# Optimization experiments

Measured on AMD Instinct MI355X. Metric: run time of the kernel, lower is better.

Reference implementation:

```python
import jax, jax.numpy as jnp
import numpy as np
import math

# ---- module hyperparams (from init_kwargs) ----
L = 10            # number of hash-grid levels
DIM = 4           # features per level
LOG2T = 16
T = 1 << LOG2T    # hash table size per level
BASE = 16         # base resolution
PLS = 2.0         # per_level_scale
SCALE_MULTI = 0.5
HID = 64
IN_DIM = L * DIM  # 40
OUT_DIM = 13      # 1 + 12
N = 1_000_000

# growth factor b = exp((ln(finest) - ln(base)) / (L - 1)), finest = base * pls**L
B_GROWTH = math.exp((math.log(BASE * PLS ** L) - math.log(BASE)) / (L - 1))
RES = [int(math.floor(BASE * B_GROWTH ** l)) for l in range(L)]

PRIMES = np.array([1, 2654435761, 805459861], dtype=np.uint32)
# 8 corner offsets of a voxel
OFFS = np.array([[i, j, k] for i in (0, 1) for j in (0, 1) for k in (0, 1)], dtype=np.uint32)


def _hash_coords(c):
    # c: uint32 [N, 8, 3] -> int32 [N, 8] indices into table of size T
    p = jnp.asarray(PRIMES)
    h = (c[..., 0] * p[0]) ^ (c[..., 1] * p[1]) ^ (c[..., 2] * p[2])
    return (h & jnp.uint32(T - 1)).astype(jnp.int32)


def _encode(x, tables):
    # x: [N,3] in [0,1]; tables: [L, T, DIM] -> [N, DIM, L]
    offs_u = jnp.asarray(OFFS)                      # uint32 [8,3]
    offs_b = jnp.asarray(OFFS.astype(bool))         # bool   [8,3]
    feats = []
    for l in range(L):
        xs = x * RES[l]
        bottom = jnp.floor(xs)
        frac = xs - bottom                          # [N,3]
        corners = bottom.astype(jnp.uint32)[:, None, :] + offs_u[None]  # [N,8,3]
        idx = _hash_coords(corners)                 # [N,8]
        cf = tables[l][idx]                         # [N,8,DIM] gather
        # trilinear weights: prod over dims of frac (if offset==1) else (1-frac)
        w = jnp.prod(jnp.where(offs_b[None], frac[:, None, :], 1.0 - frac[:, None, :]), axis=-1)  # [N,8]
        feats.append(jnp.einsum('nc,ncd->nd', w, cf))  # [N,DIM]
    return jnp.stack(feats, axis=-1)                # [N, DIM, L]


def setup_inputs() -> dict:
    key = jax.random.key(0)
    ks = jax.random.split(key, 10)
    x = jax.random.uniform(ks[0], (N, 3), dtype=jnp.float32)
    cr = jax.random.uniform(ks[1], (N,), dtype=jnp.float32)
    tables = jax.random.uniform(ks[2], (L, T, DIM), dtype=jnp.float32, minval=-1e-4, maxval=1e-4)
    gain = math.sqrt(2.0)  # calculate_gain('relu')

    def xavier(k, fan_in, fan_out):
        a = gain * math.sqrt(6.0 / (fan_in + fan_out))
        return jax.random.uniform(k, (fan_in, fan_out), dtype=jnp.float32, minval=-a, maxval=a)

    W1 = xavier(ks[3], IN_DIM, HID)
    b1 = jnp.zeros((HID,), jnp.float32)
    W2 = xavier(ks[4], HID, HID)
    b2 = jnp.zeros((HID,), jnp.float32)
    W3 = xavier(ks[5], HID, OUT_DIM)
    b3 = jnp.zeros((OUT_DIM,), jnp.float32)
    return {"x": x, "cr": cr, "tables": tables,
            "W1": W1, "b1": b1, "W2": W2, "b2": b2, "W3": W3, "b3": b3}


def reference(x, cr, tables, W1, b1, W2, b2, W3, b3):
    enc = _encode(x, tables)                        # [N, DIM, L]
    cr_s = cr.reshape(-1) * SCALE_MULTI             # [N]
    n = jnp.arange(L, dtype=jnp.float32).reshape(1, 1, L)
    denom = PLS * 4.0 * n * cr_s[:, None, None]     # [N,1,L]
    erf_x = 1.0 / jnp.sqrt(jnp.maximum(denom, 1e-12))  # safe_div/safe_sqrt; erf(huge)=1 at n=0
    scaling = jax.lax.erf(erf_x)
    h = (enc * scaling).reshape(-1, IN_DIM)         # [N, 40]
    h = jax.nn.selu(h @ W1 + b1)
    h = jax.nn.selu(h @ W2 + b2)
    return h @ W3 + b3                              # [N, 13]
```

## Files before the change

kernel.cpp:

```cpp
#include <hip/hip_runtime.h>
#include <cmath>

typedef unsigned int uint32;
typedef __bf16 bf16;
typedef __bf16 bf16x8 __attribute__((ext_vector_type(8)));
typedef float f32x4 __attribute__((ext_vector_type(4)));

#define LVLS 10
#define TSIZE 65536
#define TMASK 65535u
#define PRIME2 2654435761u
#define PRIME3 805459861u

#define WOFF_W1 0
#define WOFF_W2 4096
#define WOFF_W3 8192
#define W_ELEMS 9216
#define TAB_OFF 9216
#define TAB_ELEMS (LVLS * TSIZE * 4)

struct KParams { float resf[LVLS]; };

__global__ void prep_kernel(const float* __restrict__ W1, const float* __restrict__ W2,
                            const float* __restrict__ W3, const float* __restrict__ tables,
                            bf16* __restrict__ ws, int do_tab) {
  int tid = blockIdx.x * 256 + threadIdx.x;
  if (tid < W_ELEMS) {
    float v;
    if (tid < 4096) {
      int n = tid >> 6, k = tid & 63;
      v = (k < 40) ? W1[k * 64 + n] : 0.f;
    } else if (tid < 8192) {
      int t2 = tid - 4096; int n = t2 >> 6, k = t2 & 63;
      v = W2[k * 64 + n];
    } else {
      int t3 = tid - 8192; int n = t3 >> 6, k = t3 & 63;
      v = (n < 13) ? W3[k * 13 + n] : 0.f;
    }
    ws[tid] = (bf16)v;
  }
  if (do_tab) {
    int stride = gridDim.x * 256 * 4;
    for (int i4 = tid * 4; i4 < TAB_ELEMS; i4 += stride) {
      float4 v = *(const float4*)(tables + i4);
      bf16* dst = ws + TAB_OFF + i4;
      dst[0] = (bf16)v.x; dst[1] = (bf16)v.y; dst[2] = (bf16)v.z; dst[3] = (bf16)v.w;
    }
  }
}

__device__ __forceinline__ float selu_f(float v) {
  float neg = 1.6732632423543772f * expm1f(v);
  return 1.0507009873554805f * (v > 0.f ? v : neg);
}

__device__ __forceinline__ void gemm_stage(const bf16* __restrict__ Arow,
                                           const bf16* __restrict__ Bbase,
                                           const float* __restrict__ bvec,
                                           bf16* __restrict__ Hwr, int lr) {
  float bias[4];
#pragma unroll
  for (int nt = 0; nt < 4; ++nt) bias[nt] = bvec[nt * 16 + lr];
  f32x4 acc[4][4];
#pragma unroll
  for (int ms = 0; ms < 4; ++ms)
#pragma unroll
    for (int nt = 0; nt < 4; ++nt) {
      f32x4 a = {bias[nt], bias[nt], bias[nt], bias[nt]};
      acc[ms][nt] = a;
    }
  bf16x8 Bf[2][4];
#pragma unroll
  for (int ks = 0; ks < 2; ++ks)
#pragma unroll
    for (int nt = 0; nt < 4; ++nt)
      Bf[ks][nt] = *(const bf16x8*)(Bbase + nt * 1024 + ks * 32);
#pragma unroll
  for (int ks = 0; ks < 2; ++ks) {
    bf16x8 Af[4];
#pragma unroll
    for (int ms = 0; ms < 4; ++ms) Af[ms] = *(const bf16x8*)(Arow + ms * 1152 + ks * 32);
#pragma unroll
    for (int ms = 0; ms < 4; ++ms)
#pragma unroll
      for (int nt = 0; nt < 4; ++nt)
        acc[ms][nt] = __builtin_amdgcn_mfma_f32_16x16x32_bf16(Af[ms], Bf[ks][nt], acc[ms][nt], 0, 0, 0);
  }
#pragma unroll
  for (int ms = 0; ms < 4; ++ms)
#pragma unroll
    for (int nt = 0; nt < 4; ++nt)
#pragma unroll
      for (int r = 0; r < 4; ++r)
        Hwr[(ms * 16 + r) * 72 + nt * 16 + lr] = (bf16)selu_f(acc[ms][nt][r]);
}

template <bool TB>
__global__ __launch_bounds__(256, 3)
void ngp_fused(const float* __restrict__ x, const float* __restrict__ cr,
               const float* __restrict__ tables, const bf16* __restrict__ ws,
               const float* __restrict__ b1, const float* __restrict__ b2,
               const float* __restrict__ b3, float* __restrict__ out,
               int N, KParams kp) {
  __shared__ bf16 Hbuf[256 * 72];
  const int tid = threadIdx.x;
  const int n = blockIdx.x * 256 + tid;
  const bool valid = n < N;
  const int ncl = valid ? n : 0;

  const float px = x[ncl * 3 + 0];
  const float py = x[ncl * 3 + 1];
  const float pz = x[ncl * 3 + 2];
  const float crv = cr[ncl];

  float feat[40];
#pragma unroll
  for (int l = 0; l < LVLS; ++l) {
    const float rs = kp.resf[l];
    float xs = px * rs, ys = py * rs, zs = pz * rs;
    float bx = floorf(xs), by = floorf(ys), bz = floorf(zs);
    float fx = xs - bx, fy = ys - by, fz = zs - bz;
    uint32 cx = (uint32)bx, cy = (uint32)by, cz = (uint32)bz;
    uint32 hx0 = cx, hx1 = cx + 1u;
    uint32 hy0 = cy * PRIME2, hy1 = hy0 + PRIME2;
    uint32 hz0 = cz * PRIME3, hz1 = hz0 + PRIME3;
    uint32 idx[8];
    idx[0] = (hx0 ^ hy0 ^ hz0) & TMASK; idx[1] = (hx0 ^ hy0 ^ hz1) & TMASK;
    idx[2] = (hx0 ^ hy1 ^ hz0) & TMASK; idx[3] = (hx0 ^ hy1 ^ hz1) & TMASK;
    idx[4] = (hx1 ^ hy0 ^ hz0) & TMASK; idx[5] = (hx1 ^ hy0 ^ hz1) & TMASK;
    idx[6] = (hx1 ^ hy1 ^ hz0) & TMASK; idx[7] = (hx1 ^ hy1 ^ hz1) & TMASK;

    float f[8][4];
    if (TB) {
      const uint2* tb = ((const uint2*)(ws + TAB_OFF)) + l * TSIZE;
#pragma unroll
      for (int c = 0; c < 8; ++c) {
        uint2 q = tb[idx[c]];
        f[c][0] = __uint_as_float(q.x << 16);
        f[c][1] = __uint_as_float(q.x & 0xffff0000u);
        f[c][2] = __uint_as_float(q.y << 16);
        f[c][3] = __uint_as_float(q.y & 0xffff0000u);
      }
    } else {
      const float4* tb = ((const float4*)tables) + l * TSIZE;
#pragma unroll
      for (int c = 0; c < 8; ++c) {
        float4 q = tb[idx[c]];
        f[c][0] = q.x; f[c][1] = q.y; f[c][2] = q.z; f[c][3] = q.w;
      }
    }
    float wx1 = fx, wx0 = 1.f - fx, wy1 = fy, wy0 = 1.f - fy, wz1 = fz, wz0 = 1.f - fz;
    float wxy00 = wx0 * wy0, wxy01 = wx0 * wy1, wxy10 = wx1 * wy0, wxy11 = wx1 * wy1;
    float w[8] = {wxy00 * wz0, wxy00 * wz1, wxy01 * wz0, wxy01 * wz1,
                  wxy10 * wz0, wxy10 * wz1, wxy11 * wz0, wxy11 * wz1};
    float a0 = 0.f, a1 = 0.f, a2 = 0.f, a3 = 0.f;
#pragma unroll
    for (int c = 0; c < 8; ++c) {
      a0 = fmaf(w[c], f[c][0], a0);
      a1 = fmaf(w[c], f[c][1], a1);
      a2 = fmaf(w[c], f[c][2], a2);
      a3 = fmaf(w[c], f[c][3], a3);
    }
    float s = erff(rsqrtf(fmaxf(4.0f * (float)l * crv, 1e-12f)));
    feat[0 * 10 + l] = a0 * s;
    feat[1 * 10 + l] = a1 * s;
    feat[2 * 10 + l] = a2 * s;
    feat[3 * 10 + l] = a3 * s;
  }

  {
    bf16* row = Hbuf + tid * 72;
#pragma unroll
    for (int c = 0; c < 5; ++c) {
      bf16x8 v;
#pragma unroll
      for (int j = 0; j < 8; ++j) v[j] = (bf16)feat[c * 8 + j];
      *(bf16x8*)(row + c * 8) = v;
    }
    bf16x8 z;
#pragma unroll
    for (int j = 0; j < 8; ++j) z[j] = (bf16)0.f;
    *(bf16x8*)(row + 40) = z;
    *(bf16x8*)(row + 48) = z;
    *(bf16x8*)(row + 56) = z;
  }
  __syncthreads();

  const int w = tid >> 6;
  const int lane = tid & 63;
  const int lr = lane & 15;
  const int quad = lane >> 4;

  const bf16* Arow = Hbuf + (w * 64 + lr) * 72 + quad * 8;
  bf16* Hwr = Hbuf + (w * 64 + quad * 4) * 72;

  gemm_stage(Arow, ws + WOFF_W1 + lr * 64 + quad * 8, b1, Hwr, lr);
  __syncthreads();
  gemm_stage(Arow, ws + WOFF_W2 + lr * 64 + quad * 8, b2, Hwr, lr);
  __syncthreads();

  {
    float b3v = (lr < 13) ? b3[lr] : 0.f;
    f32x4 acc3[4];
#pragma unroll
    for (int ms = 0; ms < 4; ++ms) {
      f32x4 a = {b3v, b3v, b3v, b3v};
      acc3[ms] = a;
    }
    const bf16* B3b = ws + WOFF_W3 + lr * 64 + quad * 8;
    bf16x8 B3[2];
    B3[0] = *(const bf16x8*)(B3b);
    B3[1] = *(const bf16x8*)(B3b + 32);
#pragma unroll
    for (int ks = 0; ks < 2; ++ks) {
      bf16x8 Af[4];
#pragma unroll
      for (int ms = 0; ms < 4; ++ms) Af[ms] = *(const bf16x8*)(Arow + ms * 1152 + ks * 32);
#pragma unroll
      for (int ms = 0; ms < 4; ++ms)
        acc3[ms] = __builtin_amdgcn_mfma_f32_16x16x32_bf16(Af[ms], B3[ks], acc3[ms], 0, 0, 0);
    }
    const int rbase = blockIdx.x * 256 + w * 64 + quad * 4;
#pragma unroll
    for (int ms = 0; ms < 4; ++ms)
#pragma unroll
      for (int r = 0; r < 4; ++r) {
        int rowg = rbase + ms * 16 + r;
        if (lr < 13 && rowg < N) out[rowg * 13 + lr] = acc3[ms][r];
      }
  }
}

extern "C" void kernel_launch(void* const* d_in, const int* in_sizes, int n_in,
                              void* d_out, int out_size, void* d_ws, size_t ws_size,
                              hipStream_t stream) {
  const float* x      = (const float*)d_in[0];
  const float* cr     = (const float*)d_in[1];
  const float* tables = (const float*)d_in[2];
  const float* W1     = (const float*)d_in[3];
  const float* b1     = (const float*)d_in[4];
  const float* W2     = (const float*)d_in[5];
  const float* b2     = (const float*)d_in[6];
  const float* W3     = (const float*)d_in[7];
  const float* b3     = (const float*)d_in[8];
  float* out = (float*)d_out;
  const int N = in_sizes[1];

  KParams kp;
  double B = exp((log(16.0 * pow(2.0, 10.0)) - log(16.0)) / 9.0);
  for (int l = 0; l < LVLS; ++l) kp.resf[l] = (float)floor(16.0 * pow(B, (double)l));

  bf16* ws = (bf16*)d_ws;
  const bool tb = ws_size >= (size_t)(W_ELEMS + TAB_ELEMS) * sizeof(bf16);

  int prep_blocks = tb ? ((TAB_ELEMS / 4 + 255) / 256) : ((W_ELEMS + 255) / 256);
  prep_kernel<<<prep_blocks, 256, 0, stream>>>(W1, W2, W3, tables, ws, (int)tb);

  int blocks = (N + 255) / 256;
  if (tb)
    ngp_fused<true><<<blocks, 256, 0, stream>>>(x, cr, tables, ws, b1, b2, b3, out, N, kp);
  else
    ngp_fused<false><<<blocks, 256, 0, stream>>>(x, cr, tables, ws, b1, b2, b3, out, N, kp);
}
```

Before: 500.5 us.

## Quantize hash tables to int8 with per-level scales and raise occupancy

Measured after the change: 482.9 us. 3.5% less time.

```diff
diff --git a/kernel.cpp b/kernel.cpp
--- a/kernel.cpp
+++ b/kernel.cpp
@@ -16,15 +16,33 @@
 #define WOFF_W2 4096
 #define WOFF_W3 8192
 #define W_ELEMS 9216
-#define TAB_OFF 9216
-#define TAB_ELEMS (LVLS * TSIZE * 4)
+#define DQ_OFF 18432
+#define SC_OFF 18496
+#define TAB_OFF_B 18560
+#define TAB_ELEMS_F (LVLS * TSIZE * 4)
+#define WS_NEEDED ((size_t)TAB_OFF_B + (size_t)TAB_ELEMS_F)
 
 struct KParams { float resf[LVLS]; };
 
-__global__ void prep_kernel(const float* __restrict__ W1, const float* __restrict__ W2,
-                            const float* __restrict__ W3, const float* __restrict__ tables,
-                            bf16* __restrict__ ws, int do_tab) {
+__global__ void scale_kernel(const float* __restrict__ tables, unsigned* __restrict__ scales) {
   int tid = blockIdx.x * 256 + threadIdx.x;
+  int i4 = tid * 4;
+  if (i4 >= TAB_ELEMS_F) return;
+  float4 v = *(const float4*)(tables + i4);
+  float m = fmaxf(fmaxf(fabsf(v.x), fabsf(v.y)), fmaxf(fabsf(v.z), fabsf(v.w)));
+#pragma unroll
+  for (int off = 32; off; off >>= 1) m = fmaxf(m, __shfl_xor(m, off, 64));
+  if ((threadIdx.x & 63) == 0) {
+    int l = i4 >> 18;
+    atomicMax(scales + l, __float_as_uint(m));
+  }
+}
+
+__global__ void quant_kernel(const float* __restrict__ W1, const float* __restrict__ W2,
+                             const float* __restrict__ W3, const float* __restrict__ tables,
+                             char* __restrict__ ws8, int do_tab) {
+  int tid = blockIdx.x * 256 + threadIdx.x;
+  bf16* wsb = (bf16*)ws8;
   if (tid < W_ELEMS) {
     float v;
     if (tid < 4096) {
@@ -37,20 +55,32 @@
       int t3 = tid - 8192; int n = t3 >> 6, k = t3 & 63;
       v = (n < 13) ? W3[k * 13 + n] : 0.f;
     }
-    ws[tid] = (bf16)v;
+    wsb[tid] = (bf16)v;
+  }
+  const unsigned* scales = (const unsigned*)(ws8 + SC_OFF);
+  if (tid < LVLS) {
+    float s = __uint_as_float(scales[tid]);
+    ((float*)(ws8 + DQ_OFF))[tid] = s * (1.0f / 127.0f);
   }
   if (do_tab) {
-    int stride = gridDim.x * 256 * 4;
-    for (int i4 = tid * 4; i4 < TAB_ELEMS; i4 += stride) {
+    int i4 = tid * 4;
+    if (i4 < TAB_ELEMS_F) {
       float4 v = *(const float4*)(tables + i4);
-      bf16* dst = ws + TAB_OFF + i4;
-      dst[0] = (bf16)v.x; dst[1] = (bf16)v.y; dst[2] = (bf16)v.z; dst[3] = (bf16)v.w;
+      int l = i4 >> 18;
+      float s = __uint_as_float(scales[l]);
+      float r = (s > 0.f) ? 127.f / s : 0.f;
+      int q0 = (int)rintf(fminf(fmaxf(v.x * r, -127.f), 127.f));
+      int q1 = (int)rintf(fminf(fmaxf(v.y * r, -127.f), 127.f));
+      int q2 = (int)rintf(fminf(fmaxf(v.z * r, -127.f), 127.f));
+      int q3 = (int)rintf(fminf(fmaxf(v.w * r, -127.f), 127.f));
+      unsigned p = (q0 & 0xff) | ((q1 & 0xff) << 8) | ((q2 & 0xff) << 16) | ((q3 & 0xff) << 24);
+      *(unsigned*)(ws8 + TAB_OFF_B + i4) = p;
     }
   }
 }
 
 __device__ __forceinline__ float selu_f(float v) {
-  float neg = 1.6732632423543772f * expm1f(v);
+  float neg = 1.6732632423543772f * (__expf(v) - 1.0f);
   return 1.0507009873554805f * (v > 0.f ? v : neg);
 }
 
@@ -96,22 +126,22 @@
 }
 
 template <bool TB>
-__global__ __launch_bounds__(256, 3)
+__global__ __launch_bounds__(256, 4)
 void ngp_fused(const float* __restrict__ x, const float* __restrict__ cr,
-               const float* __restrict__ tables, const bf16* __restrict__ ws,
+               const float* __restrict__ tables, const char* __restrict__ ws8,
                const float* __restrict__ b1, const float* __restrict__ b2,
                const float* __restrict__ b3, float* __restrict__ out,
                int N, KParams kp) {
   __shared__ bf16 Hbuf[256 * 72];
   const int tid = threadIdx.x;
   const int n = blockIdx.x * 256 + tid;
-  const bool valid = n < N;
-  const int ncl = valid ? n : 0;
+  const int ncl = (n < N) ? n : 0;
 
   const float px = x[ncl * 3 + 0];
   const float py = x[ncl * 3 + 1];
   const float pz = x[ncl * 3 + 2];
   const float crv = cr[ncl];
+  const float* dq = (const float*)(ws8 + DQ_OFF);
 
   float feat[40];
 #pragma unroll
@@ -132,14 +162,14 @@
 
     float f[8][4];
     if (TB) {
-      const uint2* tb = ((const uint2*)(ws + TAB_OFF)) + l * TSIZE;
+      const unsigned* tb = ((const unsigned*)(ws8 + TAB_OFF_B)) + l * TSIZE;
 #pragma unroll
       for (int c = 0; c < 8; ++c) {
-        uint2 q = tb[idx[c]];
-        f[c][0] = __uint_as_float(q.x << 16);
-        f[c][1] = __uint_as_float(q.x & 0xffff0000u);
-        f[c][2] = __uint_as_float(q.y << 16);
-        f[c][3] = __uint_as_float(q.y & 0xffff0000u);
+        unsigned q = tb[idx[c]];
+        f[c][0] = (float)(signed char)(q & 0xff);
+        f[c][1] = (float)(signed char)((q >> 8) & 0xff);
+        f[c][2] = (float)(signed char)((q >> 16) & 0xff);
+        f[c][3] = (float)(signed char)(q >> 24);
       }
     } else {
       const float4* tb = ((const float4*)tables) + l * TSIZE;
@@ -162,6 +192,7 @@
       a3 = fmaf(w[c], f[c][3], a3);
     }
     float s = erff(rsqrtf(fmaxf(4.0f * (float)l * crv, 1e-12f)));
+    if (TB) s *= dq[l];
     feat[0 * 10 + l] = a0 * s;
     feat[1 * 10 + l] = a1 * s;
     feat[2 * 10 + l] = a2 * s;
@@ -190,13 +221,14 @@
   const int lane = tid & 63;
   const int lr = lane & 15;
   const int quad = lane >> 4;
+  const bf16* wsb = (const bf16*)ws8;
 
   const bf16* Arow = Hbuf + (w * 64 + lr) * 72 + quad * 8;
   bf16* Hwr = Hbuf + (w * 64 + quad * 4) * 72;
 
-  gemm_stage(Arow, ws + WOFF_W1 + lr * 64 + quad * 8, b1, Hwr, lr);
+  gemm_stage(Arow, wsb + WOFF_W1 + lr * 64 + quad * 8, b1, Hwr, lr);
   __syncthreads();
-  gemm_stage(Arow, ws + WOFF_W2 + lr * 64 + quad * 8, b2, Hwr, lr);
+  gemm_stage(Arow, wsb + WOFF_W2 + lr * 64 + quad * 8, b2, Hwr, lr);
   __syncthreads();
 
   {
@@ -207,7 +239,7 @@
       f32x4 a = {b3v, b3v, b3v, b3v};
       acc3[ms] = a;
     }
-    const bf16* B3b = ws + WOFF_W3 + lr * 64 + quad * 8;
+    const bf16* B3b = wsb + WOFF_W3 + lr * 64 + quad * 8;
     bf16x8 B3[2];
     B3[0] = *(const bf16x8*)(B3b);
     B3[1] = *(const bf16x8*)(B3b + 32);
@@ -250,15 +282,21 @@
   double B = exp((log(16.0 * pow(2.0, 10.0)) - log(16.0)) / 9.0);
   for (int l = 0; l < LVLS; ++l) kp.resf[l] = (float)floor(16.0 * pow(B, (double)l));
 
-  bf16* ws = (bf16*)d_ws;
-  const bool tb = ws_size >= (size_t)(W_ELEMS + TAB_ELEMS) * sizeof(bf16);
-
-  int prep_blocks = tb ? ((TAB_ELEMS / 4 + 255) / 256) : ((W_ELEMS + 255) / 256);
-  prep_kernel<<<prep_blocks, 256, 0, stream>>>(W1, W2, W3, tables, ws, (int)tb);
+  char* ws8 = (char*)d_ws;
+  const bool tb = ws_size >= WS_NEEDED;
+
+  const int qblocks = (TAB_ELEMS_F / 4 + 255) / 256;
+  if (tb) {
+    hipMemsetAsync(ws8 + SC_OFF, 0, 64, stream);
+    scale_kernel<<<qblocks, 256, 0, stream>>>(tables, (unsigned*)(ws8 + SC_OFF));
+    quant_kernel<<<qblocks, 256, 0, stream>>>(W1, W2, W3, tables, ws8, 1);
+  } else {
+    quant_kernel<<<(W_ELEMS + 255) / 256, 256, 0, stream>>>(W1, W2, W3, tables, ws8, 0);
+  }
 
   int blocks = (N + 255) / 256;
   if (tb)
-    ngp_fused<true><<<blocks, 256, 0, stream>>>(x, cr, tables, ws, b1, b2, b3, out, N, kp);
+    ngp_fused<true><<<blocks, 256, 0, stream>>>(x, cr, tables, ws8, b1, b2, b3, out, N, kp);
   else
-    ngp_fused<false><<<blocks, 256, 0, stream>>>(x, cr, tables, ws, b1, b2, b3, out, N, kp);
-}
+    ngp_fused<false><<<blocks, 256, 0, stream>>>(x, cr, tables, ws8, b1, b2, b3, out, N, kp);
+}
```
